# Performance work log

Hardware: AMD Instinct MI355X
Metric: run time of the kernel (lower is better)

The kernel has to match this reference:

```python
import jax, jax.numpy as jnp
import numpy as np

N, IN_DIM, HEADS, C = 100000, 128, 4, 32  # out_dim = HEADS*C = 128
E = 1600000


def setup_inputs() -> dict:
    key = jax.random.key(0)
    ks = jax.random.split(key, 9)
    x = jax.random.normal(ks[0], (N, IN_DIM), dtype=jnp.float32)
    edge_index = jax.random.randint(ks[1], (2, E), 0, N, dtype=jnp.int64)
    # GATConv params
    W = jax.random.normal(ks[2], (HEADS * C, IN_DIM), dtype=jnp.float32) * (1.0 / np.sqrt(IN_DIM))
    att_src = jax.random.normal(ks[3], (HEADS, C), dtype=jnp.float32) * 0.1
    att_dst = jax.random.normal(ks[4], (HEADS, C), dtype=jnp.float32) * 0.1
    bias = jax.random.normal(ks[5], (HEADS * C,), dtype=jnp.float32) * 0.01
    # complex phase + LayerNorm params
    phase = jax.random.normal(ks[6], (HEADS * C,), dtype=jnp.float32) * 0.02
    gamma = 1.0 + jax.random.normal(ks[7], (HEADS * C,), dtype=jnp.float32) * 0.01
    beta = jax.random.normal(ks[8], (HEADS * C,), dtype=jnp.float32) * 0.01
    return {"x": x, "edge_index": edge_index, "W": W, "att_src": att_src,
            "att_dst": att_dst, "bias": bias, "phase": phase, "gamma": gamma, "beta": beta}


def reference(x, edge_index, W, att_src, att_dst, bias, phase, gamma, beta):
    src, dst = edge_index[0], edge_index[1]
    h = (x @ W.T).reshape(N, HEADS, C)                      # [N,H,C]
    a_src = jnp.einsum('nhc,hc->nh', h, att_src)            # [N,H]
    a_dst = jnp.einsum('nhc,hc->nh', h, att_dst)
    e = jax.nn.leaky_relu(a_src[src] + a_dst[dst], 0.2)     # [E,H]
    # segment softmax over destination nodes (numerically stable)
    m = jax.ops.segment_max(e, dst, num_segments=N)         # [N,H]
    ex = jnp.exp(e - m[dst])
    s = jax.ops.segment_sum(ex, dst, num_segments=N)        # [N,H]
    alpha = ex / (s[dst] + 1e-16)                           # [E,H]
    msg = h[src] * alpha[:, :, None]                        # [E,H,C]
    out = jax.ops.segment_sum(msg, dst, num_segments=N).reshape(N, HEADS * C) + bias
    # complex phase magnitude: sqrt((h cos p)^2 + (h sin p)^2 + eps)
    mag = jnp.sqrt((out * jnp.cos(phase)) ** 2 + (out * jnp.sin(phase)) ** 2 + 1e-12)
    # LayerNorm
    mu = mag.mean(-1, keepdims=True)
    var = ((mag - mu) ** 2).mean(-1, keepdims=True)
    hn = (mag - mu) / jnp.sqrt(var + 1e-5) * gamma + beta
    return jax.nn.gelu(hn, approximate=False)
```

## Files before the change

kernel.cpp:

```cpp
#include <hip/hip_runtime.h>
#include <hip/hip_bf16.h>

#define N_ 100000
#define E_ 1600000
#define D_ 128
#define H_ 4
#define C_ 32
#define XSTR 136
#define NSCAT 128
#define E_CHUNK 12500
#define PARTS 782
#define NP 128
#define EBUF 2560
#define NLIN 640

using bf16 = __hip_bfloat16;
typedef __attribute__((ext_vector_type(8))) short short8;
typedef __attribute__((ext_vector_type(4))) float f32x4;
typedef __attribute__((ext_vector_type(2))) float f32x2;

__device__ __forceinline__ float u2f(unsigned u) { return __uint_as_float(u); }
__device__ __forceinline__ unsigned short f2bu(float v) {
  bf16 t = __float2bfloat16(v);
  return *(unsigned short*)&t;
}

__global__ __launch_bounds__(256) void k_histo(const int* __restrict__ ei,
                                               int* __restrict__ count) {
  __shared__ int hist[PARTS];
  const int b = blockIdx.x, tid = threadIdx.x;
  for (int i = tid; i < PARTS; i += 256) hist[i] = 0;
  __syncthreads();
  const int base = b * E_CHUNK;
  for (int i = tid; i < E_CHUNK; i += 256) {
    const int d = ei[E_ + base + i];
    atomicAdd(&hist[d >> 7], 1);
  }
  __syncthreads();
  for (int p = tid; p < PARTS; p += 256) count[p * NSCAT + b] = hist[p];
}

__global__ __launch_bounds__(1024) void k_scan(int* __restrict__ count,
                                               int* __restrict__ part_ptr) {
  __shared__ int ps[1024];
  const int p = threadIdx.x;
  int sum = 0;
  if (p < PARTS)
    for (int b = 0; b < NSCAT; b++) sum += count[p * NSCAT + b];
  ps[p] = (p < PARTS) ? sum : 0;
  __syncthreads();
  for (int off = 1; off < 1024; off <<= 1) {
    const int v = (p >= off) ? ps[p - off] : 0;
    __syncthreads();
    ps[p] += v;
    __syncthreads();
  }
  if (p < PARTS) {
    const int excl = ps[p] - sum;
    part_ptr[p] = excl;
    int run = excl;
    for (int b = 0; b < NSCAT; b++) {
      const int c = count[p * NSCAT + b];
      count[p * NSCAT + b] = run;
      run += c;
    }
  }
  if (p == 0) part_ptr[PARTS] = E_;
}

__global__ __launch_bounds__(256) void k_scatter_linear(
    const float* __restrict__ x, const float* __restrict__ W,
    const float* __restrict__ att_src, const float* __restrict__ att_dst,
    const int* __restrict__ ei, const int* __restrict__ base,
    int* __restrict__ eout, bf16* __restrict__ h,
    float* __restrict__ a_src, float* __restrict__ a_dst) {
  __shared__ unsigned short WB[16384];
  __shared__ unsigned short XS[64 * XSTR];
  __shared__ float ats[128], atd[128];
  const int tid = threadIdx.x;
  const int bid = blockIdx.x;

  if (bid < NSCAT) {
    int* lbase = (int*)WB;
    const int b = bid;
    for (int p = tid; p < PARTS; p += 256) lbase[p] = base[p * NSCAT + b];
    __syncthreads();
    const int ebase = b * E_CHUNK;
    for (int i = tid; i < E_CHUNK; i += 256) {
      const int e = ebase + i;
      const int s = ei[e];
      const int d = ei[E_ + e];
      const int pos = atomicAdd(&lbase[d >> 7], 1);
      eout[pos] = s | ((d & 127) << 20);
    }
    return;
  }

  const int lb = bid - NSCAT;
  const int lane = tid & 63, w = tid >> 6;
  const int n15 = lane & 15, quad = lane >> 4;

  for (int i = tid; i < 16384; i += 256) {
    const int n = i >> 7, k = i & 127;
    const int kk = k >> 5, q = (k >> 3) & 3, j = k & 7;
    const int frag = kk * 8 + (n >> 4);
    WB[frag * 512 + q * 128 + (n & 15) * 8 + j] = f2bu(W[n * 128 + k]);
  }
  if (tid < 128) { ats[tid] = att_src[tid]; atd[tid] = att_dst[tid]; }
  __syncthreads();

  const int nrb = (N_ + 63) / 64;
  for (int rb = lb; rb < nrb; rb += NLIN) {
    const int row0 = rb * 64;
    const int arow = row0 + w * 16 + n15;

    short8 af[4];
#pragma unroll
    for (int kk = 0; kk < 4; kk++) {
      float4 p = make_float4(0.f, 0.f, 0.f, 0.f);
      float4 q = make_float4(0.f, 0.f, 0.f, 0.f);
      if (arow < N_) {
        const float* xp = &x[(size_t)arow * 128 + kk * 32 + quad * 8];
        p = *(const float4*)xp;
        q = *(const float4*)(xp + 4);
      }
      short8 a;
      a[0] = f2bu(p.x); a[1] = f2bu(p.y); a[2] = f2bu(p.z); a[3] = f2bu(p.w);
      a[4] = f2bu(q.x); a[5] = f2bu(q.y); a[6] = f2bu(q.z); a[7] = f2bu(q.w);
      af[kk] = a;
    }

    f32x4 acc[8] = {};
#pragma unroll
    for (int kk = 0; kk < 4; kk++)
#pragma unroll
      for (int t = 0; t < 8; t++) {
        const short8 bfr = *(const short8*)&WB[(kk * 8 + t) * 512 + lane * 8];
        acc[t] = __builtin_amdgcn_mfma_f32_16x16x32_bf16(af[kk], bfr, acc[t], 0, 0, 0);
      }

#pragma unroll
    for (int t = 0; t < 8; t++)
#pragma unroll
      for (int reg = 0; reg < 4; reg++)
        XS[(w * 16 + quad * 4 + reg) * XSTR + t * 16 + n15] = f2bu(acc[t][reg]);

    const int lrow = lane >> 2, hd = lane & 3, cb = hd * 32;
    const int grow = row0 + w * 16 + lrow;
    if (grow < N_) {
      float ps = 0.f, pd = 0.f;
#pragma unroll
      for (int g = 0; g < 4; g++) {
        const uint4 v = *(const uint4*)&XS[(w * 16 + lrow) * XSTR + cb + g * 8];
        *(uint4*)&h[(size_t)grow * 128 + cb + g * 8] = v;
        const unsigned uu[4] = {v.x, v.y, v.z, v.w};
#pragma unroll
        for (int p2 = 0; p2 < 4; p2++) {
          const float f0 = u2f(uu[p2] << 16);
          const float f1 = u2f(uu[p2] & 0xffff0000u);
          const int cc = cb + g * 8 + p2 * 2;
          ps = fmaf(f0, ats[cc], ps);  ps = fmaf(f1, ats[cc + 1], ps);
          pd = fmaf(f0, atd[cc], pd);  pd = fmaf(f1, atd[cc + 1], pd);
        }
      }
      a_src[grow * 4 + hd] = ps;
      a_dst[grow * 4 + hd] = pd;
    }
  }
}

__global__ __launch_bounds__(256) void k_sortpart(
    const int* __restrict__ part_ptr, const int* __restrict__ eout,
    int* __restrict__ srcsorted, int* __restrict__ nodeptr,
    int* __restrict__ degN) {
  __shared__ int ebuf[EBUF];
  __shared__ int lsrc[EBUF];
  __shared__ int lcnt[NP], loff[NP], lptr[NP], ls[NP];
  const int p = blockIdx.x, tid = threadIdx.x;
  const int lo = part_ptr[p];
  int ne = part_ptr[p + 1] - lo;
  if (ne > EBUF) ne = EBUF;

  for (int i = tid; i < ne; i += 256) ebuf[i] = eout[lo + i];
  for (int n = tid; n < NP; n += 256) { lcnt[n] = 0; loff[n] = 0; }
  __syncthreads();
  for (int i = tid; i < ne; i += 256) atomicAdd(&lcnt[ebuf[i] >> 20], 1);
  __syncthreads();
  if (tid < NP) ls[tid] = lcnt[tid];
  __syncthreads();
  for (int off = 1; off < NP; off <<= 1) {
    const int v = (tid < NP && tid >= off) ? ls[tid - off] : 0;
    __syncthreads();
    if (tid < NP) ls[tid] += v;
    __syncthreads();
  }
  if (tid < NP) lptr[tid] = ls[tid] - lcnt[tid];
  __syncthreads();
  for (int i = tid; i < ne; i += 256) {
    const int v = ebuf[i];
    const int n = v >> 20;
    const int off = atomicAdd(&loff[n], 1);
    lsrc[lptr[n] + off] = v & 0x1FFFF;
  }
  __syncthreads();
  for (int i = tid; i < ne; i += 256) srcsorted[lo + i] = lsrc[i];
  if (tid < NP) {
    const int g = p * NP + tid;
    if (g < N_) { nodeptr[g] = lo + lptr[tid]; degN[g] = lcnt[tid]; }
  }
}

__global__ __launch_bounds__(256) void k_gather(
    const int* __restrict__ nodeptr, const int* __restrict__ degN,
    const int* __restrict__ srcsorted,
    const float* __restrict__ a_src, const float* __restrict__ a_dst,
    const bf16* __restrict__ h, const float* __restrict__ bias,
    const float* __restrict__ gamma, const float* __restrict__ beta,
    float* __restrict__ out) {
  const int lane = threadIdx.x & 63;
  const int d = blockIdx.x * 4 + (threadIdx.x >> 6);
  if (d >= N_) return;
  const int head = lane >> 4;
  const int ch = lane * 2;
  const int deg0 = degN[d];
  const int deg = deg0 < 64 ? deg0 : 64;
  const int ptr = nodeptr[d];
  const float ad = a_dst[d * 4 + head];

  int my_src = 0;
  if (lane < deg) my_src = srcsorted[ptr + lane];

  float acc0 = 0.f, acc1 = 0.f, sumw = 0.f;

  int j = 0;
  for (; j + 4 <= deg; j += 4) {
    const int s0 = __builtin_amdgcn_readlane(my_src, j);
    const int s1 = __builtin_amdgcn_readlane(my_src, j + 1);
    const int s2 = __builtin_amdgcn_readlane(my_src, j + 2);
    const int s3 = __builtin_amdgcn_readlane(my_src, j + 3);
    const float as0 = a_src[s0 * 4 + head];
    const float as1 = a_src[s1 * 4 + head];
    const float as2 = a_src[s2 * 4 + head];
    const float as3 = a_src[s3 * 4 + head];
    const unsigned h0 = *(const unsigned*)&h[((size_t)s0 << 7) + ch];
    const unsigned h1 = *(const unsigned*)&h[((size_t)s1 << 7) + ch];
    const unsigned h2 = *(const unsigned*)&h[((size_t)s2 << 7) + ch];
    const unsigned h3 = *(const unsigned*)&h[((size_t)s3 << 7) + ch];
    float e0 = as0 + ad; e0 = (e0 > 0.f) ? e0 : 0.2f * e0;
    float e1 = as1 + ad; e1 = (e1 > 0.f) ? e1 : 0.2f * e1;
    float e2 = as2 + ad; e2 = (e2 > 0.f) ? e2 : 0.2f * e2;
    float e3 = as3 + ad; e3 = (e3 > 0.f) ? e3 : 0.2f * e3;
    const float w0 = __expf(e0), w1 = __expf(e1);
    const float w2 = __expf(e2), w3 = __expf(e3);
    sumw += w0; sumw += w1; sumw += w2; sumw += w3;
    acc0 = fmaf(w0, u2f(h0 << 16), acc0); acc1 = fmaf(w0, u2f(h0 & 0xffff0000u), acc1);
    acc0 = fmaf(w1, u2f(h1 << 16), acc0); acc1 = fmaf(w1, u2f(h1 & 0xffff0000u), acc1);
    acc0 = fmaf(w2, u2f(h2 << 16), acc0); acc1 = fmaf(w2, u2f(h2 & 0xffff0000u), acc1);
    acc0 = fmaf(w3, u2f(h3 << 16), acc0); acc1 = fmaf(w3, u2f(h3 & 0xffff0000u), acc1);
  }
  for (; j < deg; ++j) {
    const int s = __builtin_amdgcn_readlane(my_src, j);
    const float as = a_src[s * 4 + head];
    const unsigned hv = *(const unsigned*)&h[((size_t)s << 7) + ch];
    float ev = as + ad;
    ev = (ev > 0.f) ? ev : 0.2f * ev;
    const float wv = __expf(ev);
    sumw += wv;
    acc0 = fmaf(wv, u2f(hv << 16), acc0);
    acc1 = fmaf(wv, u2f(hv & 0xffff0000u), acc1);
  }

  const float inv = 1.0f / (sumw + 1e-16f);
  const float2 bi = *(const float2*)&bias[ch];
  const float v0 = acc0 * inv + bi.x;
  const float v1 = acc1 * inv + bi.y;
  const float m0i = sqrtf(v0 * v0 + 1e-12f);
  const float m1i = sqrtf(v1 * v1 + 1e-12f);

  float s1r = m0i + m1i;
#pragma unroll
  for (int off = 32; off > 0; off >>= 1) s1r += __shfl_xor(s1r, off);
  const float mu = s1r * (1.0f / 128.0f);
  const float d0 = m0i - mu, d1 = m1i - mu;
  float q = d0 * d0 + d1 * d1;
#pragma unroll
  for (int off = 32; off > 0; off >>= 1) q += __shfl_xor(q, off);
  const float rstd = rsqrtf(q * (1.0f / 128.0f) + 1e-5f);
  const float2 ga = *(const float2*)&gamma[ch];
  const float2 be = *(const float2*)&beta[ch];
  const float hn0 = d0 * rstd * ga.x + be.x;
  const float hn1 = d1 * rstd * ga.y + be.y;
  const float g0 = 0.5f * hn0 * (1.0f + erff(hn0 * 0.70710678118654752f));
  const float g1 = 0.5f * hn1 * (1.0f + erff(hn1 * 0.70710678118654752f));
  f32x2 gv; gv.x = g0; gv.y = g1;
  __builtin_nontemporal_store(gv, (f32x2*)&out[(size_t)d * 128 + ch]);
}

extern "C" void kernel_launch(void* const* d_in, const int* in_sizes, int n_in,
                              void* d_out, int out_size, void* d_ws, size_t ws_size,
                              hipStream_t stream) {
  const float* x       = (const float*)d_in[0];
  const int*   ei      = (const int*)d_in[1];
  const float* W       = (const float*)d_in[2];
  const float* att_src = (const float*)d_in[3];
  const float* att_dst = (const float*)d_in[4];
  const float* bias    = (const float*)d_in[5];
  const float* gamma   = (const float*)d_in[7];
  const float* beta    = (const float*)d_in[8];
  float* out = (float*)d_out;

  bf16*  h         = (bf16*)d_ws;
  float* a_src     = (float*)(h + (size_t)N_ * D_);
  float* a_dst     = a_src + (size_t)N_ * H_;
  int*   count     = (int*)(a_dst + (size_t)N_ * H_);
  int*   part_ptr  = count + 784 * NSCAT;
  int*   eout      = part_ptr + 800;
  int*   srcsorted = eout + (size_t)E_;
  int*   nodeptr   = srcsorted + (size_t)E_;
  int*   degN      = nodeptr + (size_t)N_;

  k_histo<<<NSCAT, 256, 0, stream>>>(ei, count);
  k_scan<<<1, 1024, 0, stream>>>(count, part_ptr);
  k_scatter_linear<<<NSCAT + NLIN, 256, 0, stream>>>(x, W, att_src, att_dst,
                                                     ei, count, eout, h,
                                                     a_src, a_dst);
  k_sortpart<<<PARTS, 256, 0, stream>>>(part_ptr, eout, srcsorted, nodeptr, degN);
  k_gather<<<(N_ + 3) / 4, 256, 0, stream>>>(nodeptr, degN, srcsorted, a_src,
                                             a_dst, h, bias, gamma, beta, out);
}
```

Before: 299.3 us.

## Overlap histogram with linear, parallelize scan, precompute edge weights during sort

Fuses the destination histogram into the linear/projection kernel, replacing the previous fusion of scatter with linear. The single-block serial scan becomes a two-pass multi-block flat scan over 256 scatter chunks. Per-edge attention weights (leaky-relu plus exp for all four heads) are computed once in the partition sort kernel and stored as float4, so the gather only reads precomputed weights instead of random a_src lookups and exps. This costs an extra 25.6 MB edge-weight write and read, plus one more kernel launch.

```diff
diff --git a/kernel.cpp b/kernel.cpp
--- a/kernel.cpp
+++ b/kernel.cpp
@@ -7,12 +7,14 @@
 #define H_ 4
 #define C_ 32
 #define XSTR 136
-#define NSCAT 128
-#define E_CHUNK 12500
+#define NSCAT 256
+#define E_CHUNK 6250
 #define PARTS 782
 #define NP 128
 #define EBUF 2560
-#define NLIN 640
+#define NLIN 512
+#define FLAT (PARTS * NSCAT)
+#define SCB 196
 
 using bf16 = __hip_bfloat16;
 typedef __attribute__((ext_vector_type(8))) short short8;
@@ -25,78 +27,31 @@
   return *(unsigned short*)&t;
 }
 
-__global__ __launch_bounds__(256) void k_histo(const int* __restrict__ ei,
-                                               int* __restrict__ count) {
-  __shared__ int hist[PARTS];
-  const int b = blockIdx.x, tid = threadIdx.x;
-  for (int i = tid; i < PARTS; i += 256) hist[i] = 0;
-  __syncthreads();
-  const int base = b * E_CHUNK;
-  for (int i = tid; i < E_CHUNK; i += 256) {
-    const int d = ei[E_ + base + i];
-    atomicAdd(&hist[d >> 7], 1);
-  }
-  __syncthreads();
-  for (int p = tid; p < PARTS; p += 256) count[p * NSCAT + b] = hist[p];
-}
-
-__global__ __launch_bounds__(1024) void k_scan(int* __restrict__ count,
-                                               int* __restrict__ part_ptr) {
-  __shared__ int ps[1024];
-  const int p = threadIdx.x;
-  int sum = 0;
-  if (p < PARTS)
-    for (int b = 0; b < NSCAT; b++) sum += count[p * NSCAT + b];
-  ps[p] = (p < PARTS) ? sum : 0;
-  __syncthreads();
-  for (int off = 1; off < 1024; off <<= 1) {
-    const int v = (p >= off) ? ps[p - off] : 0;
-    __syncthreads();
-    ps[p] += v;
-    __syncthreads();
-  }
-  if (p < PARTS) {
-    const int excl = ps[p] - sum;
-    part_ptr[p] = excl;
-    int run = excl;
-    for (int b = 0; b < NSCAT; b++) {
-      const int c = count[p * NSCAT + b];
-      count[p * NSCAT + b] = run;
-      run += c;
-    }
-  }
-  if (p == 0) part_ptr[PARTS] = E_;
-}
-
-__global__ __launch_bounds__(256) void k_scatter_linear(
+__global__ __launch_bounds__(256) void k_linear_histo(
     const float* __restrict__ x, const float* __restrict__ W,
     const float* __restrict__ att_src, const float* __restrict__ att_dst,
-    const int* __restrict__ ei, const int* __restrict__ base,
-    int* __restrict__ eout, bf16* __restrict__ h,
-    float* __restrict__ a_src, float* __restrict__ a_dst) {
+    const int* __restrict__ ei, int* __restrict__ count,
+    bf16* __restrict__ h, float* __restrict__ a_src, float* __restrict__ a_dst) {
   __shared__ unsigned short WB[16384];
   __shared__ unsigned short XS[64 * XSTR];
   __shared__ float ats[128], atd[128];
   const int tid = threadIdx.x;
   const int bid = blockIdx.x;
 
-  if (bid < NSCAT) {
-    int* lbase = (int*)WB;
-    const int b = bid;
-    for (int p = tid; p < PARTS; p += 256) lbase[p] = base[p * NSCAT + b];
-    __syncthreads();
-    const int ebase = b * E_CHUNK;
-    for (int i = tid; i < E_CHUNK; i += 256) {
-      const int e = ebase + i;
-      const int s = ei[e];
-      const int d = ei[E_ + e];
-      const int pos = atomicAdd(&lbase[d >> 7], 1);
-      eout[pos] = s | ((d & 127) << 20);
-    }
+  if (bid >= NLIN) {
+    int* hist = (int*)WB;
+    const int b = bid - NLIN;
+    for (int i = tid; i < PARTS; i += 256) hist[i] = 0;
+    __syncthreads();
+    const int base = b * E_CHUNK;
+    for (int i = tid; i < E_CHUNK; i += 256)
+      atomicAdd(&hist[ei[E_ + base + i] >> 7], 1);
+    __syncthreads();
+    for (int p = tid; p < PARTS; p += 256) count[p * NSCAT + b] = hist[p];
     return;
   }
 
-  const int lb = bid - NSCAT;
+  const int lb = bid;
   const int lane = tid & 63, w = tid >> 6;
   const int n15 = lane & 15, quad = lane >> 4;
 
@@ -169,10 +124,60 @@
   }
 }
 
-__global__ __launch_bounds__(256) void k_sortpart(
-    const int* __restrict__ part_ptr, const int* __restrict__ eout,
-    int* __restrict__ srcsorted, int* __restrict__ nodeptr,
-    int* __restrict__ degN) {
+__global__ __launch_bounds__(1024) void k_scanA(int* __restrict__ count,
+                                                int* __restrict__ bsum) {
+  __shared__ int ps[1024];
+  const int g = blockIdx.x, t = threadIdx.x;
+  const int idx = g * 1024 + t;
+  const int v = (idx < FLAT) ? count[idx] : 0;
+  ps[t] = v;
+  __syncthreads();
+  for (int off = 1; off < 1024; off <<= 1) {
+    const int add = (t >= off) ? ps[t - off] : 0;
+    __syncthreads();
+    ps[t] += add;
+    __syncthreads();
+  }
+  if (idx < FLAT) count[idx] = ps[t] - v;
+  if (t == 1023) bsum[g] = ps[t];
+}
+
+__global__ __launch_bounds__(1024) void k_scanB(int* __restrict__ count,
+                                                const int* __restrict__ bsum,
+                                                int* __restrict__ part_ptr) {
+  const int g = blockIdx.x, t = threadIdx.x;
+  int off = 0;
+  for (int i = 0; i < g; i++) off += bsum[i];
+  const int idx = g * 1024 + t;
+  if (idx < FLAT) {
+    const int val = count[idx] + off;
+    count[idx] = val;
+    if ((idx & (NSCAT - 1)) == 0) part_ptr[idx / NSCAT] = val;
+  }
+  if (g == SCB - 1 && t == 1023) part_ptr[PARTS] = E_;
+}
+
+__global__ __launch_bounds__(256) void k_scatter(const int* __restrict__ ei,
+                                                 const int* __restrict__ base,
+                                                 int* __restrict__ eout) {
+  __shared__ int lbase[PARTS];
+  const int b = blockIdx.x, tid = threadIdx.x;
+  for (int p = tid; p < PARTS; p += 256) lbase[p] = base[p * NSCAT + b];
+  __syncthreads();
+  const int ebase = b * E_CHUNK;
+  for (int i = tid; i < E_CHUNK; i += 256) {
+    const int e = ebase + i;
+    const int s = ei[e];
+    const int d = ei[E_ + e];
+    const int pos = atomicAdd(&lbase[d >> 7], 1);
+    eout[pos] = s | ((d & 127) << 20);
+  }
+}
+
+__global__ __launch_bounds__(256) void k_sortw(
+    const int* __restrict__ part_ptr, int* __restrict__ eout,
+    const float* __restrict__ a_src, const float* __restrict__ a_dst,
+    float* __restrict__ ew, int* __restrict__ nodeptr, int* __restrict__ degN) {
   __shared__ int ebuf[EBUF];
   __shared__ int lsrc[EBUF];
   __shared__ int lcnt[NP], loff[NP], lptr[NP], ls[NP];
@@ -199,11 +204,23 @@
   for (int i = tid; i < ne; i += 256) {
     const int v = ebuf[i];
     const int n = v >> 20;
+    const int s = v & 0x1FFFF;
     const int off = atomicAdd(&loff[n], 1);
-    lsrc[lptr[n] + off] = v & 0x1FFFF;
-  }
-  __syncthreads();
-  for (int i = tid; i < ne; i += 256) srcsorted[lo + i] = lsrc[i];
+    const int pos = lptr[n] + off;
+    lsrc[pos] = s;
+    const int d = p * NP + n;
+    const float4 asv = *(const float4*)&a_src[s * 4];
+    const float4 adv = *(const float4*)&a_dst[d * 4];
+    float e0 = asv.x + adv.x; e0 = (e0 > 0.f) ? e0 : 0.2f * e0;
+    float e1 = asv.y + adv.y; e1 = (e1 > 0.f) ? e1 : 0.2f * e1;
+    float e2 = asv.z + adv.z; e2 = (e2 > 0.f) ? e2 : 0.2f * e2;
+    float e3 = asv.w + adv.w; e3 = (e3 > 0.f) ? e3 : 0.2f * e3;
+    float4 wv;
+    wv.x = __expf(e0); wv.y = __expf(e1); wv.z = __expf(e2); wv.w = __expf(e3);
+    *(float4*)&ew[(size_t)(lo + pos) * 4] = wv;
+  }
+  __syncthreads();
+  for (int i = tid; i < ne; i += 256) eout[lo + i] = lsrc[i];
   if (tid < NP) {
     const int g = p * NP + tid;
     if (g < N_) { nodeptr[g] = lo + lptr[tid]; degN[g] = lcnt[tid]; }
@@ -212,8 +229,7 @@
 
 __global__ __launch_bounds__(256) void k_gather(
     const int* __restrict__ nodeptr, const int* __restrict__ degN,
-    const int* __restrict__ srcsorted,
-    const float* __restrict__ a_src, const float* __restrict__ a_dst,
+    const int* __restrict__ srcsorted, const float* __restrict__ ew,
     const bf16* __restrict__ h, const float* __restrict__ bias,
     const float* __restrict__ gamma, const float* __restrict__ beta,
     float* __restrict__ out) {
@@ -225,7 +241,7 @@
   const int deg0 = degN[d];
   const int deg = deg0 < 64 ? deg0 : 64;
   const int ptr = nodeptr[d];
-  const float ad = a_dst[d * 4 + head];
+  const float* __restrict__ ewp = ew + (size_t)ptr * 4;
 
   int my_src = 0;
   if (lane < deg) my_src = srcsorted[ptr + lane];
@@ -238,21 +254,15 @@
     const int s1 = __builtin_amdgcn_readlane(my_src, j + 1);
     const int s2 = __builtin_amdgcn_readlane(my_src, j + 2);
     const int s3 = __builtin_amdgcn_readlane(my_src, j + 3);
-    const float as0 = a_src[s0 * 4 + head];
-    const float as1 = a_src[s1 * 4 + head];
-    const float as2 = a_src[s2 * 4 + head];
-    const float as3 = a_src[s3 * 4 + head];
+    const float w0 = ewp[(j + 0) * 4 + head];
+    const float w1 = ewp[(j + 1) * 4 + head];
+    const float w2 = ewp[(j + 2) * 4 + head];
+    const float w3 = ewp[(j + 3) * 4 + head];
     const unsigned h0 = *(const unsigned*)&h[((size_t)s0 << 7) + ch];
     const unsigned h1 = *(const unsigned*)&h[((size_t)s1 << 7) + ch];
     const unsigned h2 = *(const unsigned*)&h[((size_t)s2 << 7) + ch];
     const unsigned h3 = *(const unsigned*)&h[((size_t)s3 << 7) + ch];
-    float e0 = as0 + ad; e0 = (e0 > 0.f) ? e0 : 0.2f * e0;
-    float e1 = as1 + ad; e1 = (e1 > 0.f) ? e1 : 0.2f * e1;
-    float e2 = as2 + ad; e2 = (e2 > 0.f) ? e2 : 0.2f * e2;
-    float e3 = as3 + ad; e3 = (e3 > 0.f) ? e3 : 0.2f * e3;
-    const float w0 = __expf(e0), w1 = __expf(e1);
-    const float w2 = __expf(e2), w3 = __expf(e3);
-    sumw += w0; sumw += w1; sumw += w2; sumw += w3;
+    sumw += w0 + w1 + w2 + w3;
     acc0 = fmaf(w0, u2f(h0 << 16), acc0); acc1 = fmaf(w0, u2f(h0 & 0xffff0000u), acc1);
     acc0 = fmaf(w1, u2f(h1 << 16), acc0); acc1 = fmaf(w1, u2f(h1 & 0xffff0000u), acc1);
     acc0 = fmaf(w2, u2f(h2 << 16), acc0); acc1 = fmaf(w2, u2f(h2 & 0xffff0000u), acc1);
@@ -260,11 +270,8 @@
   }
   for (; j < deg; ++j) {
     const int s = __builtin_amdgcn_readlane(my_src, j);
-    const float as = a_src[s * 4 + head];
+    const float wv = ewp[j * 4 + head];
     const unsigned hv = *(const unsigned*)&h[((size_t)s << 7) + ch];
-    float ev = as + ad;
-    ev = (ev > 0.f) ? ev : 0.2f * ev;
-    const float wv = __expf(ev);
     sumw += wv;
     acc0 = fmaf(wv, u2f(hv << 16), acc0);
     acc1 = fmaf(wv, u2f(hv & 0xffff0000u), acc1);
@@ -309,22 +316,24 @@
   const float* beta    = (const float*)d_in[8];
   float* out = (float*)d_out;
 
-  bf16*  h         = (bf16*)d_ws;
-  float* a_src     = (float*)(h + (size_t)N_ * D_);
-  float* a_dst     = a_src + (size_t)N_ * H_;
-  int*   count     = (int*)(a_dst + (size_t)N_ * H_);
-  int*   part_ptr  = count + 784 * NSCAT;
-  int*   eout      = part_ptr + 800;
-  int*   srcsorted = eout + (size_t)E_;
-  int*   nodeptr   = srcsorted + (size_t)E_;
-  int*   degN      = nodeptr + (size_t)N_;
-
-  k_histo<<<NSCAT, 256, 0, stream>>>(ei, count);
-  k_scan<<<1, 1024, 0, stream>>>(count, part_ptr);
-  k_scatter_linear<<<NSCAT + NLIN, 256, 0, stream>>>(x, W, att_src, att_dst,
-                                                     ei, count, eout, h,
-                                                     a_src, a_dst);
-  k_sortpart<<<PARTS, 256, 0, stream>>>(part_ptr, eout, srcsorted, nodeptr, degN);
-  k_gather<<<(N_ + 3) / 4, 256, 0, stream>>>(nodeptr, degN, srcsorted, a_src,
-                                             a_dst, h, bias, gamma, beta, out);
-}
+  bf16*  h        = (bf16*)d_ws;
+  float* a_src    = (float*)(h + (size_t)N_ * D_);
+  float* a_dst    = a_src + (size_t)N_ * H_;
+  int*   count    = (int*)(a_dst + (size_t)N_ * H_);
+  int*   bsum     = count + (size_t)FLAT;
+  int*   part_ptr = bsum + 256;
+  int*   eout     = part_ptr + 800;
+  float* ew       = (float*)(eout + (size_t)E_);
+  int*   nodeptr  = (int*)(ew + (size_t)E_ * 4);
+  int*   degN     = nodeptr + (size_t)N_;
+
+  k_linear_histo<<<NLIN + NSCAT, 256, 0, stream>>>(x, W, att_src, att_dst, ei,
+                                                   count, h, a_src, a_dst);
+  k_scanA<<<SCB, 1024, 0, stream>>>(count, bsum);
+  k_scanB<<<SCB, 1024, 0, stream>>>(count, bsum, part_ptr);
+  k_scatter<<<NSCAT, 256, 0, stream>>>(ei, count, eout);
+  k_sortw<<<PARTS, 256, 0, stream>>>(part_ptr, eout, a_src, a_dst, ew,
+                                     nodeptr, degN);
+  k_gather<<<(N_ + 3) / 4, 256, 0, stream>>>(nodeptr, degN, eout, ew, h,
+                                             bias, gamma, beta, out);
+}
```

Result: faster. 279.7 us (-6.6%).
